# Performance work log

Hardware: AMD Instinct MI355X
Metric: run time of the kernel (lower is better)

Reference implementation:

```python
import jax, jax.numpy as jnp
import numpy as np

N_NODES = 50000
N_EDGES = 600000
IN_C, HID_C, OUT_C = 128, 128, 64
BN_EPS = 1e-5


def setup_inputs() -> dict:
    key = jax.random.key(0)
    ks = jax.random.split(key, 12)
    return {
        "x": jax.random.normal(ks[0], (N_NODES, IN_C), dtype=jnp.float32),
        "edge_index": jax.random.randint(ks[1], (2, N_EDGES), 0, N_NODES, dtype=jnp.int64),
        "W1_l": jax.random.normal(ks[2], (IN_C, HID_C), dtype=jnp.float32) * 0.05,
        "W1_r": jax.random.normal(ks[3], (IN_C, HID_C), dtype=jnp.float32) * 0.05,
        "b1": jax.random.normal(ks[4], (HID_C,), dtype=jnp.float32) * 0.05,
        "bn_gamma": jax.random.uniform(ks[5], (HID_C,), dtype=jnp.float32) + 0.5,
        "bn_beta": jax.random.normal(ks[6], (HID_C,), dtype=jnp.float32) * 0.05,
        "bn_mean": jax.random.normal(ks[7], (HID_C,), dtype=jnp.float32) * 0.05,
        "bn_var": jax.random.uniform(ks[8], (HID_C,), dtype=jnp.float32) + 0.5,
        "W2_l": jax.random.normal(ks[9], (HID_C, OUT_C), dtype=jnp.float32) * 0.05,
        "W2_r": jax.random.normal(ks[10], (HID_C, OUT_C), dtype=jnp.float32) * 0.05,
        "b2": jax.random.normal(ks[11], (OUT_C,), dtype=jnp.float32) * 0.05,
    }


def _sage_conv(h, src, dst, n_nodes, W_l, W_r, b):
    # PyG SAGEConv (aggr='mean'): out = lin_l(mean_{j in N(i)} x_j) + lin_r(x_i)
    msg = h[src]                                           # [E, C] gather
    agg = jax.ops.segment_sum(msg, dst, num_segments=n_nodes)   # [N, C] scatter-add
    cnt = jax.ops.segment_sum(jnp.ones((src.shape[0],), h.dtype), dst,
                              num_segments=n_nodes)        # [N] in-degree
    agg = agg / jnp.maximum(cnt, 1.0)[:, None]             # mean (safe for deg 0)
    return agg @ W_l + h @ W_r + b


def reference(x, edge_index, W1_l, W1_r, b1, bn_gamma, bn_beta, bn_mean, bn_var,
              W2_l, W2_r, b2):
    src = edge_index[0]
    dst = edge_index[1]
    n = x.shape[0]
    h = _sage_conv(x, src, dst, n, W1_l, W1_r, b1)
    # BatchNorm1d in eval mode (running stats)
    h = bn_gamma * (h - bn_mean) * jax.lax.rsqrt(bn_var + BN_EPS) + bn_beta
    h = jax.nn.relu(h)
    # dropout: identity in eval mode
    return _sage_conv(h, src, dst, n, W2_l, W2_r, b2)
```

## Files before the change

kernel.cpp:

```cpp
#include <hip/hip_runtime.h>
#include <hip/hip_bf16.h>

#define N_NODES 50000
#define N_EDGES 600000
#define BN_EPS 1e-5f
#define ELL_MAX 64
#define N_BUCKETS 782
#define BUCKET_CAP 1024

#define EPT 8
#define EB_EDGES (256 * EPT)
#define N_EB ((N_EDGES + EB_EDGES - 1) / EB_EDGES)
#define N_CONV_BLK 6250
#define N_W_BLK 192
#define PREP_GRID (N_EB + N_CONV_BLK + N_W_BLK + 1)

#define N_TILES 3125
#define MM_GRID 1024

typedef short bf16x8 __attribute__((ext_vector_type(8)));
typedef float f32x4 __attribute__((ext_vector_type(4)));

__device__ __forceinline__ ushort f2bf(float f) {
    unsigned u = __float_as_uint(f);
    u += 0x7fffu + ((u >> 16) & 1u);
    return (ushort)(u >> 16);
}
__device__ __forceinline__ float bf_lo(unsigned u) { return __uint_as_float(u << 16); }
__device__ __forceinline__ float bf_hi(unsigned u) { return __uint_as_float(u & 0xffff0000u); }

__global__ __launch_bounds__(256) void zero_bcnt_kernel(int* __restrict__ bcnt) {
    int t = blockIdx.x * 256 + threadIdx.x;
    if (t < N_BUCKETS) bcnt[t] = 0;
}

__global__ __launch_bounds__(256) void prep_scatter_kernel(
    const float* __restrict__ x, const int* __restrict__ eidx,
    const float* __restrict__ W1l, const float* __restrict__ W1r,
    const float* __restrict__ W2l, const float* __restrict__ W2r,
    const float* __restrict__ gamma, const float* __restrict__ beta,
    const float* __restrict__ mean, const float* __restrict__ var,
    const float* __restrict__ b1,
    ushort* __restrict__ Xb, ushort* __restrict__ W1T, ushort* __restrict__ W2T2,
    float* __restrict__ scale_, float* __restrict__ shift_,
    int* __restrict__ bcnt, unsigned* __restrict__ bucket) {
    const int blk = blockIdx.x;
    const int tid = threadIdx.x;

    if (blk < N_EB) {
        __shared__ int lcnt[N_BUCKETS];
        __shared__ int lbase[N_BUCKETS];
        const int e0 = blk * EB_EDGES;
        const int n = (N_EDGES - e0) < EB_EDGES ? (N_EDGES - e0) : EB_EDGES;

        for (int i = tid; i < N_BUCKETS; i += 256) lcnt[i] = 0;
        __syncthreads();

        unsigned pk[EPT];
        unsigned sp[EPT / 2];
        #pragma unroll
        for (int i = 0; i < EPT; ++i) {
            int idx = i * 256 + tid;
            if (idx < n) {
                int src = eidx[e0 + idx];
                int dst = eidx[N_EDGES + e0 + idx];
                int b = dst >> 6;
                int r = atomicAdd(&lcnt[b], 1);
                pk[i] = ((unsigned)b << 17) | ((unsigned)r << 6) | (unsigned)(dst & 63);
                if (i & 1) sp[i >> 1] |= ((unsigned)src << 16);
                else       sp[i >> 1]  = (unsigned)src & 0xFFFFu;
            } else {
                pk[i] = 0xFFFFFFFFu;
            }
        }
        __syncthreads();

        for (int i = tid; i < N_BUCKETS; i += 256) {
            int c = lcnt[i];
            lbase[i] = c ? atomicAdd(&bcnt[i], c) : 0;
        }
        __syncthreads();

        #pragma unroll
        for (int i = 0; i < EPT; ++i) {
            if (pk[i] != 0xFFFFFFFFu) {
                int b = pk[i] >> 17;
                int r = (pk[i] >> 6) & 0x7FF;
                int dl = pk[i] & 63;
                unsigned src = (i & 1) ? (sp[i >> 1] >> 16) : (sp[i >> 1] & 0xFFFFu);
                int p = lbase[b] + r;
                if (p < BUCKET_CAP)
                    bucket[(size_t)b * BUCKET_CAP + p] = (src << 6) | (unsigned)dl;
            }
        }
    } else if (blk < N_EB + N_CONV_BLK) {
        int t = (blk - N_EB) * 256 + tid;
        int row = t >> 5, c4 = t & 31;
        float4 v = *(const float4*)(x + (size_t)row * 128 + c4 * 4);
        ushort4 o;
        o.x = f2bf(v.x); o.y = f2bf(v.y); o.z = f2bf(v.z); o.w = f2bf(v.w);
        *(ushort4*)(Xb + (size_t)row * 128 + c4 * 4) = o;
    } else if (blk < N_EB + N_CONV_BLK + N_W_BLK) {
        int t2 = (blk - N_EB - N_CONV_BLK) * 256 + tid;
        if (t2 < 128 * 256) {
            int c = t2 >> 8, k = t2 & 255;
            float v = (k < 128) ? W1l[k * 128 + c] : W1r[(k - 128) * 128 + c];
            W1T[c * 256 + k] = f2bf(v);
        } else {
            int t3 = t2 - 128 * 256;
            int c = t3 >> 7, k = t3 & 127;
            float v = (c < 64) ? W2l[k * 64 + c] : W2r[k * 64 + (c - 64)];
            W2T2[c * 128 + k] = f2bf(v);
        }
    } else {
        if (tid < 128) {
            int c = tid;
            float sc = gamma[c] * rsqrtf(var[c] + BN_EPS);
            scale_[c] = sc;
            shift_[c] = sc * (b1[c] - mean[c]) + beta[c];
        }
    }
}

__global__ __launch_bounds__(256) void gather1_kernel(
    const ushort* __restrict__ Xb, const unsigned* __restrict__ bucket,
    const int* __restrict__ bcnt, ushort* __restrict__ Agg) {
    __shared__ ushort lell[16 * ELL_MAX];
    __shared__ int lcnt[16];
    const int tid = threadIdx.x;
    const int bkt = blockIdx.x >> 2, q = blockIdx.x & 3;

    if (tid < 16) lcnt[tid] = 0;
    int n = bcnt[bkt];
    if (n > BUCKET_CAP) n = BUCKET_CAP;
    __syncthreads();
    for (int i = tid; i < n; i += 256) {
        unsigned u = bucket[(size_t)bkt * BUCKET_CAP + i];
        int dl = u & 63;
        if ((dl >> 4) == q) {
            int r = dl & 15;
            int p = atomicAdd(&lcnt[r], 1);
            if (p < ELL_MAX) lell[(r << 6) + p] = (ushort)(u >> 6);
        }
    }
    __syncthreads();

    const int grp = tid >> 4, lane16 = tid & 15;
    const int node = (bkt << 6) + (q << 4) + grp;
    if (node >= N_NODES) return;
    const int dg = lcnt[grp];
    const int end = dg < ELL_MAX ? dg : ELL_MAX;
    const ushort* Lp = lell + (grp << 6);
    float a0 = 0.f, a1 = 0.f, a2 = 0.f, a3 = 0.f;
    float a4 = 0.f, a5 = 0.f, a6 = 0.f, a7 = 0.f;
    int j = 0;
    for (; j + 8 <= end; j += 8) {
        ushort4 sa = *(const ushort4*)(Lp + j);
        ushort4 sb = *(const ushort4*)(Lp + j + 4);
        uint4 u0 = *(const uint4*)(Xb + ((size_t)sa.x << 7) + lane16 * 8);
        uint4 u1 = *(const uint4*)(Xb + ((size_t)sa.y << 7) + lane16 * 8);
        uint4 u2 = *(const uint4*)(Xb + ((size_t)sa.z << 7) + lane16 * 8);
        uint4 u3 = *(const uint4*)(Xb + ((size_t)sa.w << 7) + lane16 * 8);
        uint4 u4 = *(const uint4*)(Xb + ((size_t)sb.x << 7) + lane16 * 8);
        uint4 u5 = *(const uint4*)(Xb + ((size_t)sb.y << 7) + lane16 * 8);
        uint4 u6 = *(const uint4*)(Xb + ((size_t)sb.z << 7) + lane16 * 8);
        uint4 u7 = *(const uint4*)(Xb + ((size_t)sb.w << 7) + lane16 * 8);
        a0 += bf_lo(u0.x) + bf_lo(u1.x) + bf_lo(u2.x) + bf_lo(u3.x)
            + bf_lo(u4.x) + bf_lo(u5.x) + bf_lo(u6.x) + bf_lo(u7.x);
        a1 += bf_hi(u0.x) + bf_hi(u1.x) + bf_hi(u2.x) + bf_hi(u3.x)
            + bf_hi(u4.x) + bf_hi(u5.x) + bf_hi(u6.x) + bf_hi(u7.x);
        a2 += bf_lo(u0.y) + bf_lo(u1.y) + bf_lo(u2.y) + bf_lo(u3.y)
            + bf_lo(u4.y) + bf_lo(u5.y) + bf_lo(u6.y) + bf_lo(u7.y);
        a3 += bf_hi(u0.y) + bf_hi(u1.y) + bf_hi(u2.y) + bf_hi(u3.y)
            + bf_hi(u4.y) + bf_hi(u5.y) + bf_hi(u6.y) + bf_hi(u7.y);
        a4 += bf_lo(u0.z) + bf_lo(u1.z) + bf_lo(u2.z) + bf_lo(u3.z)
            + bf_lo(u4.z) + bf_lo(u5.z) + bf_lo(u6.z) + bf_lo(u7.z);
        a5 += bf_hi(u0.z) + bf_hi(u1.z) + bf_hi(u2.z) + bf_hi(u3.z)
            + bf_hi(u4.z) + bf_hi(u5.z) + bf_hi(u6.z) + bf_hi(u7.z);
        a6 += bf_lo(u0.w) + bf_lo(u1.w) + bf_lo(u2.w) + bf_lo(u3.w)
            + bf_lo(u4.w) + bf_lo(u5.w) + bf_lo(u6.w) + bf_lo(u7.w);
        a7 += bf_hi(u0.w) + bf_hi(u1.w) + bf_hi(u2.w) + bf_hi(u3.w)
            + bf_hi(u4.w) + bf_hi(u5.w) + bf_hi(u6.w) + bf_hi(u7.w);
    }
    for (; j + 4 <= end; j += 4) {
        ushort4 sa = *(const ushort4*)(Lp + j);
        uint4 u0 = *(const uint4*)(Xb + ((size_t)sa.x << 7) + lane16 * 8);
        uint4 u1 = *(const uint4*)(Xb + ((size_t)sa.y << 7) + lane16 * 8);
        uint4 u2 = *(const uint4*)(Xb + ((size_t)sa.z << 7) + lane16 * 8);
        uint4 u3 = *(const uint4*)(Xb + ((size_t)sa.w << 7) + lane16 * 8);
        a0 += bf_lo(u0.x) + bf_lo(u1.x) + bf_lo(u2.x) + bf_lo(u3.x);
        a1 += bf_hi(u0.x) + bf_hi(u1.x) + bf_hi(u2.x) + bf_hi(u3.x);
        a2 += bf_lo(u0.y) + bf_lo(u1.y) + bf_lo(u2.y) + bf_lo(u3.y);
        a3 += bf_hi(u0.y) + bf_hi(u1.y) + bf_hi(u2.y) + bf_hi(u3.y);
        a4 += bf_lo(u0.z) + bf_lo(u1.z) + bf_lo(u2.z) + bf_lo(u3.z);
        a5 += bf_hi(u0.z) + bf_hi(u1.z) + bf_hi(u2.z) + bf_hi(u3.z);
        a6 += bf_lo(u0.w) + bf_lo(u1.w) + bf_lo(u2.w) + bf_lo(u3.w);
        a7 += bf_hi(u0.w) + bf_hi(u1.w) + bf_hi(u2.w) + bf_hi(u3.w);
    }
    for (; j < end; ++j) {
        int s = Lp[j];
        uint4 u = *(const uint4*)(Xb + ((size_t)s << 7) + lane16 * 8);
        a0 += bf_lo(u.x); a1 += bf_hi(u.x);
        a2 += bf_lo(u.y); a3 += bf_hi(u.y);
        a4 += bf_lo(u.z); a5 += bf_hi(u.z);
        a6 += bf_lo(u.w); a7 += bf_hi(u.w);
    }
    float ic = 1.0f / fmaxf((float)dg, 1.0f);
    uint4 o;
    o.x = (unsigned)f2bf(a0 * ic) | ((unsigned)f2bf(a1 * ic) << 16);
    o.y = (unsigned)f2bf(a2 * ic) | ((unsigned)f2bf(a3 * ic) << 16);
    o.z = (unsigned)f2bf(a4 * ic) | ((unsigned)f2bf(a5 * ic) << 16);
    o.w = (unsigned)f2bf(a6 * ic) | ((unsigned)f2bf(a7 * ic) << 16);
    *(uint4*)(Agg + ((size_t)node << 7) + lane16 * 8) = o;
}

__global__ __launch_bounds__(256) void mm_kernel(
    const ushort* __restrict__ Agg, const ushort* __restrict__ Xb,
    const ushort* __restrict__ W1T, const ushort* __restrict__ W2T2,
    const float* __restrict__ scale_, const float* __restrict__ shift_,
    const float* __restrict__ b2,
    ushort* __restrict__ Q, float* __restrict__ R) {
    __shared__ unsigned sAd[16 * 32 * 4];
    const int tid = threadIdx.x;
    const int w = tid >> 6, l = tid & 63;
    const int wc = w << 5;
    const int lr = l & 15, lk = l >> 4;

    bf16x8 bw1[8][2];
    #pragma unroll
    for (int kk = 0; kk < 8; ++kk)
        #pragma unroll
        for (int ni = 0; ni < 2; ++ni)
            bw1[kk][ni] = *(const bf16x8*)(W1T +
                (size_t)(wc + ni * 16 + lr) * 256 + kk * 32 + lk * 8);
    bf16x8 bw2[4][2];
    #pragma unroll
    for (int kk = 0; kk < 4; ++kk)
        #pragma unroll
        for (int ni = 0; ni < 2; ++ni)
            bw2[kk][ni] = *(const bf16x8*)(W2T2 +
                (size_t)(wc + ni * 16 + lr) * 128 + kk * 32 + lk * 8);

    float4 scv[2], shv[2];
    #pragma unroll
    for (int ni = 0; ni < 2; ++ni) {
        int c0 = wc + ni * 16 + lk * 4;
        scv[ni] = *(const float4*)(scale_ + c0);
        shv[ni] = *(const float4*)(shift_ + c0);
    }

    const bf16x8* sA8 = (const bf16x8*)sAd;
    const int sr = tid >> 4, sg0 = tid & 15;
    const int sr1 = (256 + tid) >> 4 - 0;

    for (int t = blockIdx.x; t < N_TILES; t += MM_GRID) {
        const int row0 = t << 4;

        #pragma unroll
        for (int i = 0; i < 2; ++i) {
            int g = i * 256 + tid;
            int r = g >> 5, gx = g & 31;
            int row = row0 + r;
            uint4 v = make_uint4(0, 0, 0, 0);
            if (row < N_NODES) {
                const ushort* src = (gx < 16)
                    ? (Agg + ((size_t)row << 7) + gx * 8)
                    : (Xb + ((size_t)row << 7) + (gx - 16) * 8);
                v = *(const uint4*)src;
            }
            *(uint4*)&sAd[((r << 5) + (gx ^ (r & 7))) << 2] = v;
        }
        __syncthreads();

        f32x4 acc[2];
        acc[0] = (f32x4){0.f, 0.f, 0.f, 0.f};
        acc[1] = (f32x4){0.f, 0.f, 0.f, 0.f};

        #pragma unroll
        for (int kk = 0; kk < 8; ++kk) {
            bf16x8 a = sA8[(lr << 5) + ((kk * 4 + lk) ^ (lr & 7))];
            acc[0] = __builtin_amdgcn_mfma_f32_16x16x32_bf16(bw1[kk][0], a, acc[0], 0, 0, 0);
            acc[1] = __builtin_amdgcn_mfma_f32_16x16x32_bf16(bw1[kk][1], a, acc[1], 0, 0, 0);
        }
        __syncthreads();

        #pragma unroll
        for (int ni = 0; ni < 2; ++ni) {
            int c0 = wc + ni * 16 + lk * 4;
            int g = c0 >> 3;
            int sub = (c0 & 4) ? 8 : 0;
            float h0 = fmaxf(acc[ni][0] * scv[ni].x + shv[ni].x, 0.f);
            float h1 = fmaxf(acc[ni][1] * scv[ni].y + shv[ni].y, 0.f);
            float h2 = fmaxf(acc[ni][2] * scv[ni].z + shv[ni].z, 0.f);
            float h3 = fmaxf(acc[ni][3] * scv[ni].w + shv[ni].w, 0.f);
            uint2 o;
            o.x = (unsigned)f2bf(h0) | ((unsigned)f2bf(h1) << 16);
            o.y = (unsigned)f2bf(h2) | ((unsigned)f2bf(h3) << 16);
            *(uint2*)((char*)sAd + (((lr << 4) + (g ^ (lr & 7))) << 4) + sub) = o;
        }
        __syncthreads();

        f32x4 acc2[2];
        acc2[0] = (f32x4){0.f, 0.f, 0.f, 0.f};
        acc2[1] = (f32x4){0.f, 0.f, 0.f, 0.f};

        #pragma unroll
        for (int kk = 0; kk < 4; ++kk) {
            bf16x8 a = *(const bf16x8*)((const char*)sAd +
                                        (((lr << 4) + ((kk * 4 + lk) ^ (lr & 7))) << 4));
            acc2[0] = __builtin_amdgcn_mfma_f32_16x16x32_bf16(bw2[kk][0], a, acc2[0], 0, 0, 0);
            acc2[1] = __builtin_amdgcn_mfma_f32_16x16x32_bf16(bw2[kk][1], a, acc2[1], 0, 0, 0);
        }

        const int rowo = row0 + lr;
        if (rowo < N_NODES) {
            #pragma unroll
            for (int ni = 0; ni < 2; ++ni) {
                int cw = wc + ni * 16 + lk * 4;
                if (cw < 64) {
                    ushort4 o;
                    o.x = f2bf(acc2[ni][0]); o.y = f2bf(acc2[ni][1]);
                    o.z = f2bf(acc2[ni][2]); o.w = f2bf(acc2[ni][3]);
                    *(ushort4*)(Q + ((size_t)rowo << 6) + cw) = o;
                } else {
                    int c0 = cw - 64;
                    float4 bias = *(const float4*)(b2 + c0);
                    float4 o;
                    o.x = acc2[ni][0] + bias.x; o.y = acc2[ni][1] + bias.y;
                    o.z = acc2[ni][2] + bias.z; o.w = acc2[ni][3] + bias.w;
                    *(float4*)(R + ((size_t)rowo << 6) + c0) = o;
                }
            }
        }
        __syncthreads();
    }
}

__global__ __launch_bounds__(256) void finish_kernel(
    const ushort* __restrict__ Q, const float* __restrict__ R,
    const unsigned* __restrict__ bucket, const int* __restrict__ bcnt,
    float* __restrict__ out) {
    __shared__ ushort lell[16 * ELL_MAX];
    __shared__ int lcnt[16];
    const int tid = threadIdx.x;
    const int bkt = blockIdx.x >> 2, q = blockIdx.x & 3;

    if (tid < 16) lcnt[tid] = 0;
    int n = bcnt[bkt];
    if (n > BUCKET_CAP) n = BUCKET_CAP;
    __syncthreads();
    for (int i = tid; i < n; i += 256) {
        unsigned u = bucket[(size_t)bkt * BUCKET_CAP + i];
        int dl = u & 63;
        if ((dl >> 4) == q) {
            int r = dl & 15;
            int p = atomicAdd(&lcnt[r], 1);
            if (p < ELL_MAX) lell[(r << 6) + p] = (ushort)(u >> 6);
        }
    }
    __syncthreads();

    const int grp = tid >> 4, lane16 = tid & 15;
    const int node = (bkt << 6) + (q << 4) + grp;
    if (node >= N_NODES) return;
    const int dg = lcnt[grp];
    const int end = dg < ELL_MAX ? dg : ELL_MAX;
    const ushort* Lp = lell + (grp << 6);
    float a0 = 0.f, a1 = 0.f, a2 = 0.f, a3 = 0.f;
    int j = 0;
    for (; j + 8 <= end; j += 8) {
        ushort4 sa = *(const ushort4*)(Lp + j);
        ushort4 sb = *(const ushort4*)(Lp + j + 4);
        uint2 u0 = *(const uint2*)(Q + ((size_t)sa.x << 6) + lane16 * 4);
        uint2 u1 = *(const uint2*)(Q + ((size_t)sa.y << 6) + lane16 * 4);
        uint2 u2 = *(const uint2*)(Q + ((size_t)sa.z << 6) + lane16 * 4);
        uint2 u3 = *(const uint2*)(Q + ((size_t)sa.w << 6) + lane16 * 4);
        uint2 u4 = *(const uint2*)(Q + ((size_t)sb.x << 6) + lane16 * 4);
        uint2 u5 = *(const uint2*)(Q + ((size_t)sb.y << 6) + lane16 * 4);
        uint2 u6 = *(const uint2*)(Q + ((size_t)sb.z << 6) + lane16 * 4);
        uint2 u7 = *(const uint2*)(Q + ((size_t)sb.w << 6) + lane16 * 4);
        a0 += bf_lo(u0.x) + bf_lo(u1.x) + bf_lo(u2.x) + bf_lo(u3.x)
            + bf_lo(u4.x) + bf_lo(u5.x) + bf_lo(u6.x) + bf_lo(u7.x);
        a1 += bf_hi(u0.x) + bf_hi(u1.x) + bf_hi(u2.x) + bf_hi(u3.x)
            + bf_hi(u4.x) + bf_hi(u5.x) + bf_hi(u6.x) + bf_hi(u7.x);
        a2 += bf_lo(u0.y) + bf_lo(u1.y) + bf_lo(u2.y) + bf_lo(u3.y)
            + bf_lo(u4.y) + bf_lo(u5.y) + bf_lo(u6.y) + bf_lo(u7.y);
        a3 += bf_hi(u0.y) + bf_hi(u1.y) + bf_hi(u2.y) + bf_hi(u3.y)
            + bf_hi(u4.y) + bf_hi(u5.y) + bf_hi(u6.y) + bf_hi(u7.y);
    }
    for (; j + 4 <= end; j += 4) {
        ushort4 ss = *(const ushort4*)(Lp + j);
        uint2 u0 = *(const uint2*)(Q + ((size_t)ss.x << 6) + lane16 * 4);
        uint2 u1 = *(const uint2*)(Q + ((size_t)ss.y << 6) + lane16 * 4);
        uint2 u2 = *(const uint2*)(Q + ((size_t)ss.z << 6) + lane16 * 4);
        uint2 u3 = *(const uint2*)(Q + ((size_t)ss.w << 6) + lane16 * 4);
        a0 += bf_lo(u0.x) + bf_lo(u1.x) + bf_lo(u2.x) + bf_lo(u3.x);
        a1 += bf_hi(u0.x) + bf_hi(u1.x) + bf_hi(u2.x) + bf_hi(u3.x);
        a2 += bf_lo(u0.y) + bf_lo(u1.y) + bf_lo(u2.y) + bf_lo(u3.y);
        a3 += bf_hi(u0.y) + bf_hi(u1.y) + bf_hi(u2.y) + bf_hi(u3.y);
    }
    for (; j < end; ++j) {
        int s = Lp[j];
        uint2 u = *(const uint2*)(Q + ((size_t)s << 6) + lane16 * 4);
        a0 += bf_lo(u.x); a1 += bf_hi(u.x);
        a2 += bf_lo(u.y); a3 += bf_hi(u.y);
    }
    float ic = 1.0f / fmaxf((float)dg, 1.0f);
    float4 r4 = *(const float4*)(R + ((size_t)node << 6) + lane16 * 4);
    float4 o;
    o.x = a0 * ic + r4.x;
    o.y = a1 * ic + r4.y;
    o.z = a2 * ic + r4.z;
    o.w = a3 * ic + r4.w;
    *(float4*)(out + ((size_t)node << 6) + lane16 * 4) = o;
}

extern "C" void kernel_launch(void* const* d_in, const int* in_sizes, int n_in,
                              void* d_out, int out_size, void* d_ws, size_t ws_size,
                              hipStream_t stream) {
    const float* x     = (const float*)d_in[0];
    const int*   eidx  = (const int*)d_in[1];
    const float* W1_l  = (const float*)d_in[2];
    const float* W1_r  = (const float*)d_in[3];
    const float* b1    = (const float*)d_in[4];
    const float* gamma = (const float*)d_in[5];
    const float* beta  = (const float*)d_in[6];
    const float* mean  = (const float*)d_in[7];
    const float* var   = (const float*)d_in[8];
    const float* W2_l  = (const float*)d_in[9];
    const float* W2_r  = (const float*)d_in[10];
    const float* b2    = (const float*)d_in[11];
    float* out = (float*)d_out;

    char* p = (char*)d_ws;
    ushort* Xb   = (ushort*)p; p += (size_t)N_NODES * 128 * 2;
    ushort* Agg  = (ushort*)p; p += (size_t)N_NODES * 128 * 2;
    ushort* Q    = (ushort*)p; p += (size_t)N_NODES * 64 * 2;
    float*  R    = (float*)p;  p += (size_t)N_NODES * 64 * 4;
    ushort* W1T  = (ushort*)p; p += 128 * 256 * 2;
    ushort* W2T2 = (ushort*)p; p += 128 * 128 * 2;
    float* scale_ = (float*)p; p += 128 * 4;
    float* shift_ = (float*)p; p += 128 * 4;
    unsigned* bucket = (unsigned*)p; p += (size_t)N_BUCKETS * BUCKET_CAP * 4;
    int* bcnt    = (int*)p;    p += (size_t)N_BUCKETS * 4;

    zero_bcnt_kernel<<<(N_BUCKETS + 255) / 256, 256, 0, stream>>>(bcnt);

    prep_scatter_kernel<<<PREP_GRID, 256, 0, stream>>>(
        x, eidx, W1_l, W1_r, W2_l, W2_r, gamma, beta, mean, var, b1,
        Xb, W1T, W2T2, scale_, shift_, bcnt, bucket);

    gather1_kernel<<<N_BUCKETS * 4, 256, 0, stream>>>(Xb, bucket, bcnt, Agg);

    mm_kernel<<<MM_GRID, 256, 0, stream>>>(
        Agg, Xb, W1T, W2T2, scale_, shift_, b2, Q, R);

    finish_kernel<<<N_BUCKETS * 4, 256, 0, stream>>>(Q, R, bucket, bcnt, out);
}
```

Before: 91.78 us.

## Fuse layer-1 neighbor gather into the MFMA matmul kernel

Merges the separate gather kernel into the persistent matmul kernel. Each block now builds the per-node ELL list in shared memory, computes the mean-aggregated features directly into the LDS A tile, and then runs both MFMA stages. This drops the Agg workspace round trip through global memory and one kernel launch. In exchange, the gather now runs inside a 1024-block persistent grid that holds many weight registers, which may lower occupancy and latency hiding for the irregular loads. A leftover redundant load of Xb is overwritten immediately and adds wasted traffic.

```diff
diff --git a/kernel.cpp b/kernel.cpp
--- a/kernel.cpp
+++ b/kernel.cpp
@@ -7,6 +7,7 @@
 #define ELL_MAX 64
 #define N_BUCKETS 782
 #define BUCKET_CAP 1024
+#define N_QB (N_BUCKETS * 4)
 
 #define EPT 8
 #define EB_EDGES (256 * EPT)
@@ -15,8 +16,7 @@
 #define N_W_BLK 192
 #define PREP_GRID (N_EB + N_CONV_BLK + N_W_BLK + 1)
 
-#define N_TILES 3125
-#define MM_GRID 1024
+#define GMM_GRID 1024
 
 typedef short bf16x8 __attribute__((ext_vector_type(8)));
 typedef float f32x4 __attribute__((ext_vector_type(4)));
@@ -122,109 +122,21 @@
     }
 }
 
-__global__ __launch_bounds__(256) void gather1_kernel(
+__global__ __launch_bounds__(256) void gmm_kernel(
     const ushort* __restrict__ Xb, const unsigned* __restrict__ bucket,
-    const int* __restrict__ bcnt, ushort* __restrict__ Agg) {
-    __shared__ ushort lell[16 * ELL_MAX];
-    __shared__ int lcnt[16];
-    const int tid = threadIdx.x;
-    const int bkt = blockIdx.x >> 2, q = blockIdx.x & 3;
-
-    if (tid < 16) lcnt[tid] = 0;
-    int n = bcnt[bkt];
-    if (n > BUCKET_CAP) n = BUCKET_CAP;
-    __syncthreads();
-    for (int i = tid; i < n; i += 256) {
-        unsigned u = bucket[(size_t)bkt * BUCKET_CAP + i];
-        int dl = u & 63;
-        if ((dl >> 4) == q) {
-            int r = dl & 15;
-            int p = atomicAdd(&lcnt[r], 1);
-            if (p < ELL_MAX) lell[(r << 6) + p] = (ushort)(u >> 6);
-        }
-    }
-    __syncthreads();
-
-    const int grp = tid >> 4, lane16 = tid & 15;
-    const int node = (bkt << 6) + (q << 4) + grp;
-    if (node >= N_NODES) return;
-    const int dg = lcnt[grp];
-    const int end = dg < ELL_MAX ? dg : ELL_MAX;
-    const ushort* Lp = lell + (grp << 6);
-    float a0 = 0.f, a1 = 0.f, a2 = 0.f, a3 = 0.f;
-    float a4 = 0.f, a5 = 0.f, a6 = 0.f, a7 = 0.f;
-    int j = 0;
-    for (; j + 8 <= end; j += 8) {
-        ushort4 sa = *(const ushort4*)(Lp + j);
-        ushort4 sb = *(const ushort4*)(Lp + j + 4);
-        uint4 u0 = *(const uint4*)(Xb + ((size_t)sa.x << 7) + lane16 * 8);
-        uint4 u1 = *(const uint4*)(Xb + ((size_t)sa.y << 7) + lane16 * 8);
-        uint4 u2 = *(const uint4*)(Xb + ((size_t)sa.z << 7) + lane16 * 8);
-        uint4 u3 = *(const uint4*)(Xb + ((size_t)sa.w << 7) + lane16 * 8);
-        uint4 u4 = *(const uint4*)(Xb + ((size_t)sb.x << 7) + lane16 * 8);
-        uint4 u5 = *(const uint4*)(Xb + ((size_t)sb.y << 7) + lane16 * 8);
-        uint4 u6 = *(const uint4*)(Xb + ((size_t)sb.z << 7) + lane16 * 8);
-        uint4 u7 = *(const uint4*)(Xb + ((size_t)sb.w << 7) + lane16 * 8);
-        a0 += bf_lo(u0.x) + bf_lo(u1.x) + bf_lo(u2.x) + bf_lo(u3.x)
-            + bf_lo(u4.x) + bf_lo(u5.x) + bf_lo(u6.x) + bf_lo(u7.x);
-        a1 += bf_hi(u0.x) + bf_hi(u1.x) + bf_hi(u2.x) + bf_hi(u3.x)
-            + bf_hi(u4.x) + bf_hi(u5.x) + bf_hi(u6.x) + bf_hi(u7.x);
-        a2 += bf_lo(u0.y) + bf_lo(u1.y) + bf_lo(u2.y) + bf_lo(u3.y)
-            + bf_lo(u4.y) + bf_lo(u5.y) + bf_lo(u6.y) + bf_lo(u7.y);
-        a3 += bf_hi(u0.y) + bf_hi(u1.y) + bf_hi(u2.y) + bf_hi(u3.y)
-            + bf_hi(u4.y) + bf_hi(u5.y) + bf_hi(u6.y) + bf_hi(u7.y);
-        a4 += bf_lo(u0.z) + bf_lo(u1.z) + bf_lo(u2.z) + bf_lo(u3.z)
-            + bf_lo(u4.z) + bf_lo(u5.z) + bf_lo(u6.z) + bf_lo(u7.z);
-        a5 += bf_hi(u0.z) + bf_hi(u1.z) + bf_hi(u2.z) + bf_hi(u3.z)
-            + bf_hi(u4.z) + bf_hi(u5.z) + bf_hi(u6.z) + bf_hi(u7.z);
-        a6 += bf_lo(u0.w) + bf_lo(u1.w) + bf_lo(u2.w) + bf_lo(u3.w)
-            + bf_lo(u4.w) + bf_lo(u5.w) + bf_lo(u6.w) + bf_lo(u7.w);
-        a7 += bf_hi(u0.w) + bf_hi(u1.w) + bf_hi(u2.w) + bf_hi(u3.w)
-            + bf_hi(u4.w) + bf_hi(u5.w) + bf_hi(u6.w) + bf_hi(u7.w);
-    }
-    for (; j + 4 <= end; j += 4) {
-        ushort4 sa = *(const ushort4*)(Lp + j);
-        uint4 u0 = *(const uint4*)(Xb + ((size_t)sa.x << 7) + lane16 * 8);
-        uint4 u1 = *(const uint4*)(Xb + ((size_t)sa.y << 7) + lane16 * 8);
-        uint4 u2 = *(const uint4*)(Xb + ((size_t)sa.z << 7) + lane16 * 8);
-        uint4 u3 = *(const uint4*)(Xb + ((size_t)sa.w << 7) + lane16 * 8);
-        a0 += bf_lo(u0.x) + bf_lo(u1.x) + bf_lo(u2.x) + bf_lo(u3.x);
-        a1 += bf_hi(u0.x) + bf_hi(u1.x) + bf_hi(u2.x) + bf_hi(u3.x);
-        a2 += bf_lo(u0.y) + bf_lo(u1.y) + bf_lo(u2.y) + bf_lo(u3.y);
-        a3 += bf_hi(u0.y) + bf_hi(u1.y) + bf_hi(u2.y) + bf_hi(u3.y);
-        a4 += bf_lo(u0.z) + bf_lo(u1.z) + bf_lo(u2.z) + bf_lo(u3.z);
-        a5 += bf_hi(u0.z) + bf_hi(u1.z) + bf_hi(u2.z) + bf_hi(u3.z);
-        a6 += bf_lo(u0.w) + bf_lo(u1.w) + bf_lo(u2.w) + bf_lo(u3.w);
-        a7 += bf_hi(u0.w) + bf_hi(u1.w) + bf_hi(u2.w) + bf_hi(u3.w);
-    }
-    for (; j < end; ++j) {
-        int s = Lp[j];
-        uint4 u = *(const uint4*)(Xb + ((size_t)s << 7) + lane16 * 8);
-        a0 += bf_lo(u.x); a1 += bf_hi(u.x);
-        a2 += bf_lo(u.y); a3 += bf_hi(u.y);
-        a4 += bf_lo(u.z); a5 += bf_hi(u.z);
-        a6 += bf_lo(u.w); a7 += bf_hi(u.w);
-    }
-    float ic = 1.0f / fmaxf((float)dg, 1.0f);
-    uint4 o;
-    o.x = (unsigned)f2bf(a0 * ic) | ((unsigned)f2bf(a1 * ic) << 16);
-    o.y = (unsigned)f2bf(a2 * ic) | ((unsigned)f2bf(a3 * ic) << 16);
-    o.z = (unsigned)f2bf(a4 * ic) | ((unsigned)f2bf(a5 * ic) << 16);
-    o.w = (unsigned)f2bf(a6 * ic) | ((unsigned)f2bf(a7 * ic) << 16);
-    *(uint4*)(Agg + ((size_t)node << 7) + lane16 * 8) = o;
-}
-
-__global__ __launch_bounds__(256) void mm_kernel(
-    const ushort* __restrict__ Agg, const ushort* __restrict__ Xb,
+    const int* __restrict__ bcnt,
     const ushort* __restrict__ W1T, const ushort* __restrict__ W2T2,
     const float* __restrict__ scale_, const float* __restrict__ shift_,
     const float* __restrict__ b2,
     ushort* __restrict__ Q, float* __restrict__ R) {
     __shared__ unsigned sAd[16 * 32 * 4];
+    __shared__ ushort lell[16 * ELL_MAX];
+    __shared__ int lcnt[16];
     const int tid = threadIdx.x;
     const int w = tid >> 6, l = tid & 63;
     const int wc = w << 5;
     const int lr = l & 15, lk = l >> 4;
+    const int grp = tid >> 4, lane16 = tid & 15;
 
     bf16x8 bw1[8][2];
     #pragma unroll
@@ -240,7 +152,6 @@
         for (int ni = 0; ni < 2; ++ni)
             bw2[kk][ni] = *(const bf16x8*)(W2T2 +
                 (size_t)(wc + ni * 16 + lr) * 128 + kk * 32 + lk * 8);
-
     float4 scv[2], shv[2];
     #pragma unroll
     for (int ni = 0; ni < 2; ++ni) {
@@ -250,32 +161,111 @@
     }
 
     const bf16x8* sA8 = (const bf16x8*)sAd;
-    const int sr = tid >> 4, sg0 = tid & 15;
-    const int sr1 = (256 + tid) >> 4 - 0;
-
-    for (int t = blockIdx.x; t < N_TILES; t += MM_GRID) {
-        const int row0 = t << 4;
-
-        #pragma unroll
-        for (int i = 0; i < 2; ++i) {
-            int g = i * 256 + tid;
-            int r = g >> 5, gx = g & 31;
-            int row = row0 + r;
+
+    for (int qb = blockIdx.x; qb < N_QB; qb += GMM_GRID) {
+        const int bkt = qb >> 2, q = qb & 3;
+        const int row0 = qb << 4;
+
+        if (tid < 16) lcnt[tid] = 0;
+        int n = bcnt[bkt];
+        if (n > BUCKET_CAP) n = BUCKET_CAP;
+
+        {
+            int row = row0 + grp;
             uint4 v = make_uint4(0, 0, 0, 0);
-            if (row < N_NODES) {
-                const ushort* src = (gx < 16)
-                    ? (Agg + ((size_t)row << 7) + gx * 8)
-                    : (Xb + ((size_t)row << 7) + (gx - 16) * 8);
-                v = *(const uint4*)src;
-            }
-            *(uint4*)&sAd[((r << 5) + (gx ^ (r & 7))) << 2] = v;
+            if (row < N_NODES)
+                v = *(const uint4*)(Xb + ((size_t)row << 7) + (lane16 + 16 - 16) * 8 + 64);
+            v = make_uint4(0, 0, 0, 0);
+            if (row < N_NODES)
+                v = *(const uint4*)(Xb + ((size_t)row << 7) + lane16 * 8 + 0);
+            int r = grp, gs = 16 + lane16;
+            *(uint4*)&sAd[((r << 5) + (gs ^ (r & 7))) << 2] = v;
+        }
+        __syncthreads();
+
+        for (int i = tid; i < n; i += 256) {
+            unsigned u = bucket[(size_t)bkt * BUCKET_CAP + i];
+            int dl = u & 63;
+            if ((dl >> 4) == q) {
+                int r = dl & 15;
+                int p = atomicAdd(&lcnt[r], 1);
+                if (p < ELL_MAX) lell[(r << 6) + p] = (ushort)(u >> 6);
+            }
+        }
+        __syncthreads();
+
+        {
+            const int dg = lcnt[grp];
+            const int end = dg < ELL_MAX ? dg : ELL_MAX;
+            const ushort* Lp = lell + (grp << 6);
+            float a0 = 0.f, a1 = 0.f, a2 = 0.f, a3 = 0.f;
+            float a4 = 0.f, a5 = 0.f, a6 = 0.f, a7 = 0.f;
+            int j = 0;
+            for (; j + 8 <= end; j += 8) {
+                ushort4 sa = *(const ushort4*)(Lp + j);
+                ushort4 sb = *(const ushort4*)(Lp + j + 4);
+                uint4 u0 = *(const uint4*)(Xb + ((size_t)sa.x << 7) + lane16 * 8);
+                uint4 u1 = *(const uint4*)(Xb + ((size_t)sa.y << 7) + lane16 * 8);
+                uint4 u2 = *(const uint4*)(Xb + ((size_t)sa.z << 7) + lane16 * 8);
+                uint4 u3 = *(const uint4*)(Xb + ((size_t)sa.w << 7) + lane16 * 8);
+                uint4 u4 = *(const uint4*)(Xb + ((size_t)sb.x << 7) + lane16 * 8);
+                uint4 u5 = *(const uint4*)(Xb + ((size_t)sb.y << 7) + lane16 * 8);
+                uint4 u6 = *(const uint4*)(Xb + ((size_t)sb.z << 7) + lane16 * 8);
+                uint4 u7 = *(const uint4*)(Xb + ((size_t)sb.w << 7) + lane16 * 8);
+                a0 += bf_lo(u0.x) + bf_lo(u1.x) + bf_lo(u2.x) + bf_lo(u3.x)
+                    + bf_lo(u4.x) + bf_lo(u5.x) + bf_lo(u6.x) + bf_lo(u7.x);
+                a1 += bf_hi(u0.x) + bf_hi(u1.x) + bf_hi(u2.x) + bf_hi(u3.x)
+                    + bf_hi(u4.x) + bf_hi(u5.x) + bf_hi(u6.x) + bf_hi(u7.x);
+                a2 += bf_lo(u0.y) + bf_lo(u1.y) + bf_lo(u2.y) + bf_lo(u3.y)
+                    + bf_lo(u4.y) + bf_lo(u5.y) + bf_lo(u6.y) + bf_lo(u7.y);
+                a3 += bf_hi(u0.y) + bf_hi(u1.y) + bf_hi(u2.y) + bf_hi(u3.y)
+                    + bf_hi(u4.y) + bf_hi(u5.y) + bf_hi(u6.y) + bf_hi(u7.y);
+                a4 += bf_lo(u0.z) + bf_lo(u1.z) + bf_lo(u2.z) + bf_lo(u3.z)
+                    + bf_lo(u4.z) + bf_lo(u5.z) + bf_lo(u6.z) + bf_lo(u7.z);
+                a5 += bf_hi(u0.z) + bf_hi(u1.z) + bf_hi(u2.z) + bf_hi(u3.z)
+                    + bf_hi(u4.z) + bf_hi(u5.z) + bf_hi(u6.z) + bf_hi(u7.z);
+                a6 += bf_lo(u0.w) + bf_lo(u1.w) + bf_lo(u2.w) + bf_lo(u3.w)
+                    + bf_lo(u4.w) + bf_lo(u5.w) + bf_lo(u6.w) + bf_lo(u7.w);
+                a7 += bf_hi(u0.w) + bf_hi(u1.w) + bf_hi(u2.w) + bf_hi(u3.w)
+                    + bf_hi(u4.w) + bf_hi(u5.w) + bf_hi(u6.w) + bf_hi(u7.w);
+            }
+            for (; j + 4 <= end; j += 4) {
+                ushort4 sa = *(const ushort4*)(Lp + j);
+                uint4 u0 = *(const uint4*)(Xb + ((size_t)sa.x << 7) + lane16 * 8);
+                uint4 u1 = *(const uint4*)(Xb + ((size_t)sa.y << 7) + lane16 * 8);
+                uint4 u2 = *(const uint4*)(Xb + ((size_t)sa.z << 7) + lane16 * 8);
+                uint4 u3 = *(const uint4*)(Xb + ((size_t)sa.w << 7) + lane16 * 8);
+                a0 += bf_lo(u0.x) + bf_lo(u1.x) + bf_lo(u2.x) + bf_lo(u3.x);
+                a1 += bf_hi(u0.x) + bf_hi(u1.x) + bf_hi(u2.x) + bf_hi(u3.x);
+                a2 += bf_lo(u0.y) + bf_lo(u1.y) + bf_lo(u2.y) + bf_lo(u3.y);
+                a3 += bf_hi(u0.y) + bf_hi(u1.y) + bf_hi(u2.y) + bf_hi(u3.y);
+                a4 += bf_lo(u0.z) + bf_lo(u1.z) + bf_lo(u2.z) + bf_lo(u3.z);
+                a5 += bf_hi(u0.z) + bf_hi(u1.z) + bf_hi(u2.z) + bf_hi(u3.z);
+                a6 += bf_lo(u0.w) + bf_lo(u1.w) + bf_lo(u2.w) + bf_lo(u3.w);
+                a7 += bf_hi(u0.w) + bf_hi(u1.w) + bf_hi(u2.w) + bf_hi(u3.w);
+            }
+            for (; j < end; ++j) {
+                int s = Lp[j];
+                uint4 u = *(const uint4*)(Xb + ((size_t)s << 7) + lane16 * 8);
+                a0 += bf_lo(u.x); a1 += bf_hi(u.x);
+                a2 += bf_lo(u.y); a3 += bf_hi(u.y);
+                a4 += bf_lo(u.z); a5 += bf_hi(u.z);
+                a6 += bf_lo(u.w); a7 += bf_hi(u.w);
+            }
+            float ic = 1.0f / fmaxf((float)dg, 1.0f);
+            uint4 o;
+            o.x = (unsigned)f2bf(a0 * ic) | ((unsigned)f2bf(a1 * ic) << 16);
+            o.y = (unsigned)f2bf(a2 * ic) | ((unsigned)f2bf(a3 * ic) << 16);
+            o.z = (unsigned)f2bf(a4 * ic) | ((unsigned)f2bf(a5 * ic) << 16);
+            o.w = (unsigned)f2bf(a6 * ic) | ((unsigned)f2bf(a7 * ic) << 16);
+            int r = grp;
+            *(uint4*)&sAd[((r << 5) + (lane16 ^ (r & 7))) << 2] = o;
         }
         __syncthreads();
 
         f32x4 acc[2];
         acc[0] = (f32x4){0.f, 0.f, 0.f, 0.f};
         acc[1] = (f32x4){0.f, 0.f, 0.f, 0.f};
-
         #pragma unroll
         for (int kk = 0; kk < 8; ++kk) {
             bf16x8 a = sA8[(lr << 5) + ((kk * 4 + lk) ^ (lr & 7))];
@@ -303,7 +293,6 @@
         f32x4 acc2[2];
         acc2[0] = (f32x4){0.f, 0.f, 0.f, 0.f};
         acc2[1] = (f32x4){0.f, 0.f, 0.f, 0.f};
-
         #pragma unroll
         for (int kk = 0; kk < 4; ++kk) {
             bf16x8 a = *(const bf16x8*)((const char*)sAd +
@@ -434,7 +423,6 @@
 
     char* p = (char*)d_ws;
     ushort* Xb   = (ushort*)p; p += (size_t)N_NODES * 128 * 2;
-    ushort* Agg  = (ushort*)p; p += (size_t)N_NODES * 128 * 2;
     ushort* Q    = (ushort*)p; p += (size_t)N_NODES * 64 * 2;
     float*  R    = (float*)p;  p += (size_t)N_NODES * 64 * 4;
     ushort* W1T  = (ushort*)p; p += 128 * 256 * 2;
@@ -450,10 +438,8 @@
         x, eidx, W1_l, W1_r, W2_l, W2_r, gamma, beta, mean, var, b1,
         Xb, W1T, W2T2, scale_, shift_, bcnt, bucket);
 
-    gather1_kernel<<<N_BUCKETS * 4, 256, 0, stream>>>(Xb, bucket, bcnt, Agg);
-
-    mm_kernel<<<MM_GRID, 256, 0, stream>>>(
-        Agg, Xb, W1T, W2T2, scale_, shift_, b2, Q, R);
+    gmm_kernel<<<GMM_GRID, 256, 0, stream>>>(
+        Xb, bucket, bcnt, W1T, W2T2, scale_, shift_, b2, Q, R);
 
     finish_kernel<<<N_BUCKETS * 4, 256, 0, stream>>>(Q, R, bucket, bcnt, out);
 }
```

After: 95.76 us. +4.3%, slower.
